# Kernel tuning notes

Hardware: AMD Instinct MI355X
Metric: run time of the kernel (lower is better)

The kernel has to match this reference:

```python
import jax, jax.numpy as jnp
import numpy as np
import math

NM = 1024
NH = 16
ND = NM // NH
B, L = 4, 1024


def setup_inputs() -> dict:
    key = jax.random.key(0)
    ks = jax.random.split(key, 11)
    s = 1.0 / math.sqrt(NM)
    return {
        "x": jax.random.normal(ks[0], (B, L, NM), dtype=jnp.float32),
        "mask": jax.random.randint(ks[1], (B, L, L), 0, 2, dtype=jnp.int32),
        "Wq": jax.random.normal(ks[2], (NM, NM), dtype=jnp.float32) * s,
        "bq": jax.random.normal(ks[3], (NM,), dtype=jnp.float32) * 0.01,
        "Wk": jax.random.normal(ks[4], (NM, NM), dtype=jnp.float32) * s,
        "bk": jax.random.normal(ks[5], (NM,), dtype=jnp.float32) * 0.01,
        "Wv": jax.random.normal(ks[6], (NM, NM), dtype=jnp.float32) * s,
        "bv": jax.random.normal(ks[7], (NM,), dtype=jnp.float32) * 0.01,
        "Wo": jax.random.normal(ks[8], (NM, NM), dtype=jnp.float32) * s,
        "bo": jax.random.normal(ks[9], (NM,), dtype=jnp.float32) * 0.01,
    }


def reference(x, mask, Wq, bq, Wk, bk, Wv, bv, Wo, bo):
    nB, nL, _ = x.shape
    m = mask.astype(x.dtype)  # [B,L,L]
    # QKV projections (torch Linear: y = x @ W.T + b)
    q = (x @ Wq.T + bq).reshape(nB, nL, NH, ND)
    k = (x @ Wk.T + bk).reshape(nB, nL, NH, ND)
    v = (x @ Wv.T + bv).reshape(nB, nL, NH, ND)
    # scaled dot product; NOTE: module scales by 1/sqrt(nM), not 1/sqrt(nD)
    scores = jnp.einsum("bqhd,bkhd->bhqk", q, k) / math.sqrt(NM)
    # additive/multiplicative padding mask: S*mask - (1-mask)*1e9
    mb = m[:, None, :, :]  # broadcast over heads [B,1,L,L]
    scores = scores * mb - (1.0 - mb) * 1e9
    attn = jax.nn.softmax(scores, axis=-1)
    ctx = jnp.einsum("bhqk,bkhd->bqhd", attn, v).reshape(nB, nL, NM)
    out = ctx @ Wo.T + bo
    return out
```

## Files before the change

### kernel.cpp

```cpp
#include <hip/hip_runtime.h>

typedef unsigned short u16;
typedef unsigned int   u32;
typedef unsigned long long u64;
typedef __attribute__((ext_vector_type(8))) short  short8;
typedef __attribute__((ext_vector_type(4))) float  floatx4;

#define NM 1024
#define NH 16
#define ND 64
#define BB 4
#define LL 1024
#define MM (BB*LL)

__device__ __forceinline__ u16 f2bf(float f) {
  union { float f; u32 u; } c; c.f = f;
  u32 u = c.u;
  return (u16)((u + 0x7fffu + ((u >> 16) & 1u)) >> 16);
}

__device__ __forceinline__ void cstore(u16* p, float v)  { *p = f2bf(v); }
__device__ __forceinline__ void cstore(float* p, float v){ *p = v; }

__device__ __forceinline__ void load_lds16(const u16* g, u16* l) {
  __builtin_amdgcn_global_load_lds((const __attribute__((address_space(1))) u32*)g,
                                   (__attribute__((address_space(3))) u32*)l,
                                   16, 0, 0);
}

__global__ void conv_f32_bf16(const float* __restrict__ src, u16* __restrict__ dst, int n) {
  int i = (blockIdx.x * blockDim.x + threadIdx.x) * 4;
  if (i < n) {
    float4 v = *(const float4*)(src + i);
    u16 o0 = f2bf(v.x), o1 = f2bf(v.y), o2 = f2bf(v.z), o3 = f2bf(v.w);
    ushort4 o; o.x = o0; o.y = o1; o.z = o2; o.w = o3;
    *(ushort4*)(dst + i) = o;
  }
}

__global__ void pack_mask(const int* __restrict__ m, u32* __restrict__ mp) {
  int i = blockIdx.x * blockDim.x + threadIdx.x;
  int v = m[i];
  u64 b = __ballot(v != 0);
  int lane = threadIdx.x & 63;
  if (lane == 0) {
    mp[(i >> 5) + 0] = (u32)b;
    mp[(i >> 5) + 1] = (u32)(b >> 32);
  }
}

template<typename OUT_T>
__global__ __launch_bounds__(256)
void gemm_bt_kernel(const u16* __restrict__ A,
                    const u16* __restrict__ Ball,
                    const float* __restrict__ b0, const float* __restrict__ b1,
                    const float* __restrict__ b2,
                    OUT_T* __restrict__ Call)
{
  constexpr int K = 1024, N = 1024;
  const int z = blockIdx.z;
  const u16* Bm = Ball + (size_t)z * N * K;
  const float* bias = (z == 0) ? b0 : ((z == 1) ? b1 : b2);
  OUT_T* C = Call + (size_t)z * MM * N;

  __shared__ u16 As[128 * 32];
  __shared__ u16 Bs[128 * 32];

  const int tid = threadIdx.x;
  const int w = tid >> 6, lane = tid & 63, lane15 = lane & 15, quad = lane >> 4;
  const int row0 = blockIdx.x * 128, col0 = blockIdx.y * 128;
  const int wm = (w >> 1) * 64, wn = (w & 1) * 64;
  const int sr = lane >> 2, sc = (lane & 3) * 8;

  floatx4 acc[4][4];
  const floatx4 zero = {0.f, 0.f, 0.f, 0.f};
  #pragma unroll
  for (int i = 0; i < 4; i++)
    #pragma unroll
    for (int j = 0; j < 4; j++) acc[i][j] = zero;

  for (int kk = 0; kk < K; kk += 32) {
    __syncthreads();
    #pragma unroll
    for (int c = 0; c < 2; c++) {
      int g = w * 2 + c;
      const u16* ga = A  + (size_t)(row0 + g * 16 + sr) * K + kk + sc;
      load_lds16(ga, &As[g * 512]);
      const u16* gb = Bm + (size_t)(col0 + g * 16 + sr) * K + kk + sc;
      load_lds16(gb, &Bs[g * 512]);
    }
    __syncthreads();

    short8 af[4], bf[4];
    #pragma unroll
    for (int i = 0; i < 4; i++)
      af[i] = *(short8*)&As[(wm + i * 16 + lane15) * 32 + quad * 8];
    #pragma unroll
    for (int j = 0; j < 4; j++)
      bf[j] = *(short8*)&Bs[(wn + j * 16 + lane15) * 32 + quad * 8];
    #pragma unroll
    for (int i = 0; i < 4; i++)
      #pragma unroll
      for (int j = 0; j < 4; j++)
        acc[i][j] = __builtin_amdgcn_mfma_f32_16x16x32_bf16(af[i], bf[j], acc[i][j], 0, 0, 0);
  }

  #pragma unroll
  for (int i = 0; i < 4; i++) {
    #pragma unroll
    for (int j = 0; j < 4; j++) {
      int col = col0 + wn + j * 16 + lane15;
      float bv = bias[col];
      #pragma unroll
      for (int r = 0; r < 4; r++) {
        int row = row0 + wm + i * 16 + quad * 4 + r;
        cstore(&C[(size_t)row * N + col], acc[i][j][r] + bv);
      }
    }
  }
}

__global__ __launch_bounds__(256)
void attn_kernel(const u16* __restrict__ Q, const u16* __restrict__ K,
                 const u16* __restrict__ V, const u32* __restrict__ mp,
                 u16* __restrict__ CTX)
{
  __shared__ u16 Qs[64 * 72];
  __shared__ u16 Ks[128 * 72];
  __shared__ u16 Vt[64 * 136];
  __shared__ u16 Ps[64 * 136];
  __shared__ u32 msk[64 * 4];
  __shared__ float l_acc[64];

  const int tid = threadIdx.x;
  const int w = tid >> 6, lane = tid & 63, lane15 = lane & 15, quad = lane >> 4;
  const int qt = blockIdx.x, bh = blockIdx.y;
  const int b = bh >> 4, h = bh & 15;
  const int q0 = qt * 64;
  const size_t qbase  = (size_t)(b * LL + q0) * NM + h * ND;
  const size_t kvbase = (size_t)(b * LL) * NM + h * ND;
  const float scale = 0.03125f;

  for (int i = tid; i < 512; i += 256) {
    int r = i >> 3, c8 = i & 7;
    *(uint4*)&Qs[r * 72 + c8 * 8] = *(const uint4*)(Q + qbase + (size_t)r * NM + c8 * 8);
  }
  if (tid < 64) l_acc[tid] = 0.f;

  const floatx4 zero = {0.f, 0.f, 0.f, 0.f};
  floatx4 o_acc[4];
  #pragma unroll
  for (int j = 0; j < 4; j++) o_acc[j] = zero;

  for (int kt = 0; kt < 8; kt++) {
    const int k0 = kt * 128;
    __syncthreads();

    for (int i = tid; i < 1024; i += 256) {
      int r = i >> 3, c8 = i & 7;
      *(uint4*)&Ks[r * 72 + c8 * 8] =
          *(const uint4*)(K + kvbase + (size_t)(k0 + r) * NM + c8 * 8);
    }
    {
      int d = tid & 63, rb = tid >> 6;
      #pragma unroll
      for (int t4 = 0; t4 < 4; t4++) {
        int kk0 = rb * 32 + t4 * 8;
        short8 vv;
        #pragma unroll
        for (int jj = 0; jj < 8; jj++)
          vv[jj] = (short)V[kvbase + (size_t)(k0 + kk0 + jj) * NM + d];
        *(short8*)&Vt[d * 136 + kk0] = vv;
      }
    }
    {
      int r = tid >> 2, w32 = tid & 3;
      msk[tid] = mp[(size_t)(b * LL + q0 + r) * 32 + (k0 >> 5) + w32];
    }
    __syncthreads();

    floatx4 s_acc[8];
    #pragma unroll
    for (int j = 0; j < 8; j++) s_acc[j] = zero;
    #pragma unroll
    for (int ks = 0; ks < 2; ks++) {
      short8 a = *(short8*)&Qs[(w * 16 + lane15) * 72 + ks * 32 + quad * 8];
      #pragma unroll
      for (int j = 0; j < 8; j++) {
        short8 bf = *(short8*)&Ks[(j * 16 + lane15) * 72 + ks * 32 + quad * 8];
        s_acc[j] = __builtin_amdgcn_mfma_f32_16x16x32_bf16(a, bf, s_acc[j], 0, 0, 0);
      }
    }

    float rsum[4] = {0.f, 0.f, 0.f, 0.f};
    #pragma unroll
    for (int j = 0; j < 8; j++) {
      int kcol = j * 16 + lane15;
      #pragma unroll
      for (int r = 0; r < 4; r++) {
        int ql = w * 16 + quad * 4 + r;
        u32 mw = msk[ql * 4 + (kcol >> 5)];
        float p = 0.f;
        if ((mw >> (kcol & 31)) & 1u) p = __expf(s_acc[j][r] * scale);
        rsum[r] += p;
        Ps[ql * 136 + kcol] = f2bf(p);
      }
    }
    #pragma unroll
    for (int r = 0; r < 4; r++) {
      float s = rsum[r];
      s += __shfl_xor(s, 1); s += __shfl_xor(s, 2);
      s += __shfl_xor(s, 4); s += __shfl_xor(s, 8);
      if (lane15 == 0) l_acc[w * 16 + quad * 4 + r] += s;
    }

    #pragma unroll
    for (int ks = 0; ks < 4; ks++) {
      short8 a = *(short8*)&Ps[(w * 16 + lane15) * 136 + ks * 32 + quad * 8];
      #pragma unroll
      for (int j = 0; j < 4; j++) {
        short8 bf = *(short8*)&Vt[(j * 16 + lane15) * 136 + ks * 32 + quad * 8];
        o_acc[j] = __builtin_amdgcn_mfma_f32_16x16x32_bf16(a, bf, o_acc[j], 0, 0, 0);
      }
    }
  }

  #pragma unroll
  for (int j = 0; j < 4; j++) {
    #pragma unroll
    for (int r = 0; r < 4; r++) {
      int ql = w * 16 + quad * 4 + r;
      float val = o_acc[j][r] / l_acc[ql];
      CTX[(size_t)(b * LL + q0 + ql) * NM + h * ND + j * 16 + lane15] = f2bf(val);
    }
  }
}

extern "C" void kernel_launch(void* const* d_in, const int* in_sizes, int n_in,
                              void* d_out, int out_size, void* d_ws, size_t ws_size,
                              hipStream_t stream) {
  const float* x  = (const float*)d_in[0];
  const int*   mk = (const int*)  d_in[1];
  const float* Wq = (const float*)d_in[2]; const float* bq = (const float*)d_in[3];
  const float* Wk = (const float*)d_in[4]; const float* bk = (const float*)d_in[5];
  const float* Wv = (const float*)d_in[6]; const float* bv = (const float*)d_in[7];
  const float* Wo = (const float*)d_in[8]; const float* bo = (const float*)d_in[9];
  float* out = (float*)d_out;

  char* ws = (char*)d_ws;
  u16* xb   = (u16*)(ws);
  u16* Wcat = (u16*)(ws + ((size_t)8  << 20));
  u16* Wob  = (u16*)(ws + ((size_t)14 << 20));
  u16* QKV  = (u16*)(ws + ((size_t)16 << 20));
  u16* CTX  = (u16*)(ws + ((size_t)40 << 20));
  u32* mp   = (u32*)(ws + ((size_t)48 << 20));

  conv_f32_bf16<<<4096, 256, 0, stream>>>(x,  xb,               MM * NM);
  conv_f32_bf16<<<1024, 256, 0, stream>>>(Wq, Wcat,             NM * NM);
  conv_f32_bf16<<<1024, 256, 0, stream>>>(Wk, Wcat + NM * NM,   NM * NM);
  conv_f32_bf16<<<1024, 256, 0, stream>>>(Wv, Wcat + 2 * NM*NM, NM * NM);
  conv_f32_bf16<<<1024, 256, 0, stream>>>(Wo, Wob,              NM * NM);
  pack_mask<<<16384, 256, 0, stream>>>(mk, mp);

  gemm_bt_kernel<u16><<<dim3(32, 8, 3), 256, 0, stream>>>(xb, Wcat, bq, bk, bv, QKV);

  attn_kernel<<<dim3(16, 64), 256, 0, stream>>>(QKV, QKV + (size_t)MM * NM,
                                                QKV + 2 * (size_t)MM * NM, mp, CTX);

  gemm_bt_kernel<float><<<dim3(32, 8, 1), 256, 0, stream>>>(CTX, Wob, bo, bo, bo, out);
}
```

Before: 245.2 us.

## Write V transposed from QKV GEMM and drop LDS staging in attention

The QKV GEMM epilogue now writes V in a transposed [d][token] layout. The attention kernel therefore reads K and V^T directly from global memory into MFMA operands, with no block-wide LDS staging or __syncthreads. Each wave keeps its own Q fragment in registers and a private P tile in LDS, and launch bounds request higher occupancy. The five fp32-to-bf16 conversion launches are merged into one. The trade-off is that the transposed V store is strided and uncoalesced, and K/V reads are no longer shared across the four waves through LDS.

```diff
diff --git a/kernel.cpp b/kernel.cpp
--- a/kernel.cpp
+++ b/kernel.cpp
@@ -28,12 +28,24 @@
                                    16, 0, 0);
 }
 
-__global__ void conv_f32_bf16(const float* __restrict__ src, u16* __restrict__ dst, int n) {
-  int i = (blockIdx.x * blockDim.x + threadIdx.x) * 4;
-  if (i < n) {
+__global__ void conv_all(const float* __restrict__ x,  const float* __restrict__ Wq,
+                         const float* __restrict__ Wk, const float* __restrict__ Wv,
+                         const float* __restrict__ Wo,
+                         u16* __restrict__ xb, u16* __restrict__ wcat, u16* __restrict__ wob) {
+  const int y = blockIdx.y;
+  const float* src; u16* dst;
+  if      (y == 0) { src = x;  dst = xb; }
+  else if (y == 1) { src = Wq; dst = wcat; }
+  else if (y == 2) { src = Wk; dst = wcat + NM * NM; }
+  else if (y == 3) { src = Wv; dst = wcat + 2 * NM * NM; }
+  else             { src = Wo; dst = wob; }
+  const int nrep = (y == 0) ? 4 : 1;
+  const int base = blockIdx.x * 256 + threadIdx.x;
+  for (int t = 0; t < nrep; t++) {
+    int i = (base + t * 262144) * 4;
     float4 v = *(const float4*)(src + i);
-    u16 o0 = f2bf(v.x), o1 = f2bf(v.y), o2 = f2bf(v.z), o3 = f2bf(v.w);
-    ushort4 o; o.x = o0; o.y = o1; o.z = o2; o.w = o3;
+    ushort4 o;
+    o.x = f2bf(v.x); o.y = f2bf(v.y); o.z = f2bf(v.z); o.w = f2bf(v.w);
     *(ushort4*)(dst + i) = o;
   }
 }
@@ -49,13 +61,14 @@
   }
 }
 
-template<typename OUT_T>
+template<typename OUT_T, bool TRANS_Z2>
 __global__ __launch_bounds__(256)
 void gemm_bt_kernel(const u16* __restrict__ A,
                     const u16* __restrict__ Ball,
                     const float* __restrict__ b0, const float* __restrict__ b1,
                     const float* __restrict__ b2,
-                    OUT_T* __restrict__ Call)
+                    OUT_T* __restrict__ Call,
+                    u16* __restrict__ VTout)
 {
   constexpr int K = 1024, N = 1024;
   const int z = blockIdx.z;
@@ -114,113 +127,99 @@
       #pragma unroll
       for (int r = 0; r < 4; r++) {
         int row = row0 + wm + i * 16 + quad * 4 + r;
-        cstore(&C[(size_t)row * N + col], acc[i][j][r] + bv);
-      }
-    }
-  }
-}
-
-__global__ __launch_bounds__(256)
+        if (TRANS_Z2 && z == 2)
+          VTout[(size_t)col * MM + row] = f2bf(acc[i][j][r] + bv);
+        else
+          cstore(&C[(size_t)row * N + col], acc[i][j][r] + bv);
+      }
+    }
+  }
+}
+
+__global__ __launch_bounds__(256, 4)
 void attn_kernel(const u16* __restrict__ Q, const u16* __restrict__ K,
-                 const u16* __restrict__ V, const u32* __restrict__ mp,
+                 const u16* __restrict__ VT, const u32* __restrict__ mp,
                  u16* __restrict__ CTX)
 {
-  __shared__ u16 Qs[64 * 72];
-  __shared__ u16 Ks[128 * 72];
-  __shared__ u16 Vt[64 * 136];
-  __shared__ u16 Ps[64 * 136];
-  __shared__ u32 msk[64 * 4];
-  __shared__ float l_acc[64];
+  __shared__ u16 Ps[4][16 * 136];
 
   const int tid = threadIdx.x;
   const int w = tid >> 6, lane = tid & 63, lane15 = lane & 15, quad = lane >> 4;
   const int qt = blockIdx.x, bh = blockIdx.y;
   const int b = bh >> 4, h = bh & 15;
-  const int q0 = qt * 64;
-  const size_t qbase  = (size_t)(b * LL + q0) * NM + h * ND;
+  const int q0 = qt * 64 + w * 16;
   const size_t kvbase = (size_t)(b * LL) * NM + h * ND;
-  const float scale = 0.03125f;
-
-  for (int i = tid; i < 512; i += 256) {
-    int r = i >> 3, c8 = i & 7;
-    *(uint4*)&Qs[r * 72 + c8 * 8] = *(const uint4*)(Q + qbase + (size_t)r * NM + c8 * 8);
-  }
-  if (tid < 64) l_acc[tid] = 0.f;
+  const size_t vtbase = (size_t)(h * ND) * MM + (size_t)b * LL;
+  u16* ps = &Ps[w][0];
+
+  short8 aq[2];
+  {
+    const u16* qp = Q + (size_t)(b * LL + q0 + lane15) * NM + h * ND + quad * 8;
+    aq[0] = *(const short8*)(qp);
+    aq[1] = *(const short8*)(qp + 32);
+  }
 
   const floatx4 zero = {0.f, 0.f, 0.f, 0.f};
-  floatx4 o_acc[4];
-  #pragma unroll
-  for (int j = 0; j < 4; j++) o_acc[j] = zero;
-
+  floatx4 o_acc[4] = {zero, zero, zero, zero};
+  float lsum[4] = {0.f, 0.f, 0.f, 0.f};
+
+  const u32* mrow = mp + (size_t)(b * LL + q0 + quad * 4) * 32;
+
+  #pragma unroll 1
   for (int kt = 0; kt < 8; kt++) {
     const int k0 = kt * 128;
-    __syncthreads();
-
-    for (int i = tid; i < 1024; i += 256) {
-      int r = i >> 3, c8 = i & 7;
-      *(uint4*)&Ks[r * 72 + c8 * 8] =
-          *(const uint4*)(K + kvbase + (size_t)(k0 + r) * NM + c8 * 8);
-    }
-    {
-      int d = tid & 63, rb = tid >> 6;
-      #pragma unroll
-      for (int t4 = 0; t4 < 4; t4++) {
-        int kk0 = rb * 32 + t4 * 8;
-        short8 vv;
+
+    uint4 m4[4];
+    #pragma unroll
+    for (int r = 0; r < 4; r++)
+      m4[r] = *(const uint4*)(mrow + r * 32 + kt * 4);
+
+    float rsum[4] = {0.f, 0.f, 0.f, 0.f};
+
+    #pragma unroll
+    for (int half = 0; half < 2; half++) {
+      floatx4 s_acc[4] = {zero, zero, zero, zero};
+      #pragma unroll
+      for (int ks = 0; ks < 2; ks++) {
         #pragma unroll
-        for (int jj = 0; jj < 8; jj++)
-          vv[jj] = (short)V[kvbase + (size_t)(k0 + kk0 + jj) * NM + d];
-        *(short8*)&Vt[d * 136 + kk0] = vv;
-      }
-    }
-    {
-      int r = tid >> 2, w32 = tid & 3;
-      msk[tid] = mp[(size_t)(b * LL + q0 + r) * 32 + (k0 >> 5) + w32];
-    }
-    __syncthreads();
-
-    floatx4 s_acc[8];
-    #pragma unroll
-    for (int j = 0; j < 8; j++) s_acc[j] = zero;
-    #pragma unroll
-    for (int ks = 0; ks < 2; ks++) {
-      short8 a = *(short8*)&Qs[(w * 16 + lane15) * 72 + ks * 32 + quad * 8];
-      #pragma unroll
-      for (int j = 0; j < 8; j++) {
-        short8 bf = *(short8*)&Ks[(j * 16 + lane15) * 72 + ks * 32 + quad * 8];
-        s_acc[j] = __builtin_amdgcn_mfma_f32_16x16x32_bf16(a, bf, s_acc[j], 0, 0, 0);
-      }
-    }
-
-    float rsum[4] = {0.f, 0.f, 0.f, 0.f};
-    #pragma unroll
-    for (int j = 0; j < 8; j++) {
-      int kcol = j * 16 + lane15;
-      #pragma unroll
-      for (int r = 0; r < 4; r++) {
-        int ql = w * 16 + quad * 4 + r;
-        u32 mw = msk[ql * 4 + (kcol >> 5)];
-        float p = 0.f;
-        if ((mw >> (kcol & 31)) & 1u) p = __expf(s_acc[j][r] * scale);
-        rsum[r] += p;
-        Ps[ql * 136 + kcol] = f2bf(p);
-      }
-    }
+        for (int j4 = 0; j4 < 4; j4++) {
+          const int j = half * 4 + j4;
+          const short8 bk = *(const short8*)(K + kvbase +
+              (size_t)(k0 + j * 16 + lane15) * NM + ks * 32 + quad * 8);
+          s_acc[j4] = __builtin_amdgcn_mfma_f32_16x16x32_bf16(aq[ks], bk, s_acc[j4], 0, 0, 0);
+        }
+      }
+      #pragma unroll
+      for (int j4 = 0; j4 < 4; j4++) {
+        const int j = half * 4 + j4;
+        const int shift = (j & 1) * 16 + lane15;
+        #pragma unroll
+        for (int r = 0; r < 4; r++) {
+          const u32 mw = ((const u32*)&m4[r])[j >> 1];
+          float p = 0.f;
+          if ((mw >> shift) & 1u) p = __expf(s_acc[j4][r] * 0.03125f);
+          rsum[r] += p;
+          ps[(quad * 4 + r) * 136 + j * 16 + lane15] = f2bf(p);
+        }
+      }
+    }
+
     #pragma unroll
     for (int r = 0; r < 4; r++) {
       float s = rsum[r];
       s += __shfl_xor(s, 1); s += __shfl_xor(s, 2);
       s += __shfl_xor(s, 4); s += __shfl_xor(s, 8);
-      if (lane15 == 0) l_acc[w * 16 + quad * 4 + r] += s;
+      lsum[r] += s;
     }
 
     #pragma unroll
     for (int ks = 0; ks < 4; ks++) {
-      short8 a = *(short8*)&Ps[(w * 16 + lane15) * 136 + ks * 32 + quad * 8];
+      const short8 a = *(const short8*)&ps[lane15 * 136 + ks * 32 + quad * 8];
       #pragma unroll
       for (int j = 0; j < 4; j++) {
-        short8 bf = *(short8*)&Vt[(j * 16 + lane15) * 136 + ks * 32 + quad * 8];
-        o_acc[j] = __builtin_amdgcn_mfma_f32_16x16x32_bf16(a, bf, o_acc[j], 0, 0, 0);
+        const short8 bv = *(const short8*)(VT + vtbase +
+            (size_t)(j * 16 + lane15) * MM + k0 + ks * 32 + quad * 8);
+        o_acc[j] = __builtin_amdgcn_mfma_f32_16x16x32_bf16(a, bv, o_acc[j], 0, 0, 0);
       }
     }
   }
@@ -229,9 +228,8 @@
   for (int j = 0; j < 4; j++) {
     #pragma unroll
     for (int r = 0; r < 4; r++) {
-      int ql = w * 16 + quad * 4 + r;
-      float val = o_acc[j][r] / l_acc[ql];
-      CTX[(size_t)(b * LL + q0 + ql) * NM + h * ND + j * 16 + lane15] = f2bf(val);
+      float val = o_acc[j][r] / lsum[r];
+      CTX[(size_t)(b * LL + q0 + quad * 4 + r) * NM + h * ND + j * 16 + lane15] = f2bf(val);
     }
   }
 }
@@ -251,21 +249,20 @@
   u16* xb   = (u16*)(ws);
   u16* Wcat = (u16*)(ws + ((size_t)8  << 20));
   u16* Wob  = (u16*)(ws + ((size_t)14 << 20));
-  u16* QKV  = (u16*)(ws + ((size_t)16 << 20));
+  u16* QKb  = (u16*)(ws + ((size_t)16 << 20));
+  u16* VT   = (u16*)(ws + ((size_t)32 << 20));
   u16* CTX  = (u16*)(ws + ((size_t)40 << 20));
   u32* mp   = (u32*)(ws + ((size_t)48 << 20));
 
-  conv_f32_bf16<<<4096, 256, 0, stream>>>(x,  xb,               MM * NM);
-  conv_f32_bf16<<<1024, 256, 0, stream>>>(Wq, Wcat,             NM * NM);
-  conv_f32_bf16<<<1024, 256, 0, stream>>>(Wk, Wcat + NM * NM,   NM * NM);
-  conv_f32_bf16<<<1024, 256, 0, stream>>>(Wv, Wcat + 2 * NM*NM, NM * NM);
-  conv_f32_bf16<<<1024, 256, 0, stream>>>(Wo, Wob,              NM * NM);
+  conv_all<<<dim3(1024, 5), 256, 0, stream>>>(x, Wq, Wk, Wv, Wo, xb, Wcat, Wob);
   pack_mask<<<16384, 256, 0, stream>>>(mk, mp);
 
-  gemm_bt_kernel<u16><<<dim3(32, 8, 3), 256, 0, stream>>>(xb, Wcat, bq, bk, bv, QKV);
-
-  attn_kernel<<<dim3(16, 64), 256, 0, stream>>>(QKV, QKV + (size_t)MM * NM,
-                                                QKV + 2 * (size_t)MM * NM, mp, CTX);
-
-  gemm_bt_kernel<float><<<dim3(32, 8, 1), 256, 0, stream>>>(CTX, Wob, bo, bo, bo, out);
-}
+  gemm_bt_kernel<u16, true><<<dim3(32, 8, 3), 256, 0, stream>>>(
+      xb, Wcat, bq, bk, bv, QKb, VT);
+
+  attn_kernel<<<dim3(16, 64), 256, 0, stream>>>(
+      QKb, QKb + (size_t)MM * NM, VT, mp, CTX);
+
+  gemm_bt_kernel<float, false><<<dim3(32, 8, 1), 256, 0, stream>>>(
+      CTX, Wob, bo, bo, bo, out, nullptr);
+}
```

After: 289.8 us. +18.2%, slower.
